# Kernel tuning notes

Measured on AMD Instinct MI355X. Metric: run time of the kernel, lower is better.

The kernel has to match this reference:

```python
import jax, jax.numpy as jnp
import numpy as np

IB = 8      # input/hidden activation bits
ABMVM = 8   # gate activation bits after MVM
ABNM = 8    # near-memory compute bits
NL = 0.05   # analog noise level
CY_DIV = 2.0
CY_SCALE = 2.0


def quant_pass(x, wb, sign):
    # Faithful port of QuantFunc.forward: clip/clamp then fake-quant (round to grid).
    if wb is None or wb == 0:
        return x
    if sign:
        delta = 0.0 if wb == 1 else 1.0 / (2.0 ** (wb - 1))
        x = jnp.clip(x, -1.0 + delta, 1.0 - delta)
    else:
        x = jnp.clip(x, 0.0, 1.0)
    if wb == 1:
        return jnp.sign(x)
    scale = 2.0 ** (wb - 1) if sign else 2.0 ** wb
    return jnp.round(x * scale) / scale


def setup_inputs() -> dict:
    key = jax.random.key(0)
    ks = jax.random.split(key, 7)
    B, I, H = 4096, 1024, 1024
    return {
        "input": jax.random.normal(ks[0], (B, I), jnp.float32),
        "hx": jax.random.normal(ks[1], (B, H), jnp.float32),
        "cx": jax.random.normal(ks[2], (B, H), jnp.float32),
        "weight_ih": jax.random.normal(ks[3], (4 * H, I), jnp.float32) * 0.1,
        "weight_hh": jax.random.normal(ks[4], (4 * H, H), jnp.float32) * 0.1,
        "bias_ih": jax.random.normal(ks[5], (4 * H,), jnp.float32) * 0.1,
        "bias_hh": jax.random.normal(ks[6], (4 * H,), jnp.float32) * 0.1,
        "train": 0,
    }


def reference(input, hx, cx, weight_ih, weight_hh, bias_ih, bias_hh, train):
    # Per-call Gaussian noise (simulated analog hardware); fixed key for reproducibility.
    nk = jax.random.split(jax.random.key(42), 4)
    noise_w_ih = jax.random.normal(nk[0], weight_ih.T.shape, weight_ih.dtype) * weight_ih.max() * NL
    noise_w_hh = jax.random.normal(nk[1], weight_hh.T.shape, weight_hh.dtype) * weight_hh.max() * NL
    noise_b_ih = jax.random.normal(nk[2], bias_ih.shape, bias_ih.dtype) * bias_ih.max() * NL
    noise_b_hh = jax.random.normal(nk[3], bias_hh.shape, bias_hh.dtype) * bias_hh.max() * NL

    # gates: [B, 4H]
    gates = (quant_pass(input, IB, True) @ (weight_ih.T + noise_w_ih) + bias_ih + noise_b_ih
             + quant_pass(hx, IB, True) @ (weight_hh.T + noise_w_hh) + bias_hh + noise_b_hh)

    ingate, forgetgate, cellgate, outgate = jnp.split(gates, 4, axis=1)
    ingate = quant_pass(jax.nn.sigmoid(ingate), ABMVM, False)
    forgetgate = quant_pass(jax.nn.sigmoid(forgetgate), ABMVM, False)
    cellgate = quant_pass(jnp.tanh(cellgate), ABMVM, True)
    outgate = quant_pass(jax.nn.sigmoid(outgate), ABMVM, False)

    cy = quant_pass((quant_pass(forgetgate * cx, ABNM, True)
                     + quant_pass(ingate * cellgate, ABNM, True)) / CY_DIV, ABNM, True)
    hy = quant_pass(outgate * quant_pass(jnp.tanh(cy * CY_SCALE), ABNM, True), ABNM, True)
    return (hy, cy)
```

## Files before the change

kernel.cpp:

```cpp
#include <hip/hip_runtime.h>
#include <hip/hip_bf16.h>
#include <stdint.h>
#include <stddef.h>


#define PART 1

typedef __attribute__((ext_vector_type(8))) short bf16x8;
typedef __attribute__((ext_vector_type(4))) float f32x4;

#define BATCH 4096

#define WS_A_OFF    ((size_t)0)
#define WS_B_OFF    ((size_t)16 << 20)
#define WS_BIAS_OFF ((size_t)48 << 20)
#define WS_MAX_OFF  (WS_BIAS_OFF + 16384)

__host__ __device__ inline void tf2x32(uint32_t k0, uint32_t k1,
                                       uint32_t x0, uint32_t x1,
                                       uint32_t &o0, uint32_t &o1)
{
  const uint32_t k2 = k0 ^ k1 ^ 0x1BD11BDAu;
#define TFR(r) { x0 += x1; x1 = (x1 << (r)) | (x1 >> (32 - (r))); x1 ^= x0; }
  x0 += k0; x1 += k1;
  TFR(13) TFR(15) TFR(26) TFR(6)
  x0 += k1; x1 += k2 + 1u;
  TFR(17) TFR(29) TFR(16) TFR(24)
  x0 += k2; x1 += k0 + 2u;
  TFR(13) TFR(15) TFR(26) TFR(6)
  x0 += k0; x1 += k1 + 3u;
  TFR(17) TFR(29) TFR(16) TFR(24)
  x0 += k1; x1 += k2 + 4u;
  TFR(13) TFR(15) TFR(26) TFR(6)
  x0 += k2; x1 += k0 + 5u;
#undef TFR
  o0 = x0; o1 = x1;
}

__device__ inline uint32_t jax_bits32(uint32_t k0, uint32_t k1, uint32_t i, uint32_t size)
{
#if PART
  uint32_t a, b;
  tf2x32(k0, k1, 0u, i, a, b);
  return a ^ b;
#else
  uint32_t half = size >> 1, a, b;
  if (i < half) { tf2x32(k0, k1, i, i + half, a, b); return a; }
  tf2x32(k0, k1, i - half, i, a, b); return b;
#endif
}

__device__ inline float bits_to_normal(uint32_t bits)
{
  float f = __uint_as_float((bits >> 9) | 0x3F800000u) - 1.0f;
  const float lo = -0x1.fffffep-1f;
  float u = fmaxf(lo, f * 2.0f + lo);
  float w = -log1pf(-u * u);
  float p;
  if (w < 5.0f) {
    w -= 2.5f;
    p = 2.81022636e-08f;
    p = fmaf(p, w, 3.43273939e-07f);
    p = fmaf(p, w, -3.5233877e-06f);
    p = fmaf(p, w, -4.39150654e-06f);
    p = fmaf(p, w, 0.00021858087f);
    p = fmaf(p, w, -0.00125372503f);
    p = fmaf(p, w, -0.00417768164f);
    p = fmaf(p, w, 0.246640727f);
    p = fmaf(p, w, 1.50140941f);
  } else {
    w = sqrtf(w) - 3.0f;
    p = -0.000200214257f;
    p = fmaf(p, w, 0.000100950558f);
    p = fmaf(p, w, 0.00134934322f);
    p = fmaf(p, w, -0.00367342844f);
    p = fmaf(p, w, 0.00573950773f);
    p = fmaf(p, w, -0.0076224613f);
    p = fmaf(p, w, 0.00943887047f);
    p = fmaf(p, w, 1.00167406f);
    p = fmaf(p, w, 2.83297682f);
  }
  return 0x1.6a09e6p+0f * (p * u);
}

__device__ inline float quantS8(float x)
{
  x = fminf(fmaxf(x, -0.9921875f), 0.9921875f);
  return rintf(x * 128.0f) * 0.0078125f;
}
__device__ inline float quantU8(float x)
{
  x = fminf(fmaxf(x, 0.0f), 1.0f);
  return rintf(x * 256.0f) * 0.00390625f;
}

#define LOG2E 1.44269504088896340736f
__device__ inline float sigmoid_fast(float x)
{
  float e = __builtin_amdgcn_exp2f(x * -LOG2E);
  return __builtin_amdgcn_rcpf(1.0f + e);
}
__device__ inline float tanh_fast(float x)
{
  float a = fabsf(x);
  float e = __builtin_amdgcn_exp2f(a * (-2.0f * LOG2E));
  float t = (1.0f - e) * __builtin_amdgcn_rcpf(1.0f + e);
  return copysignf(t, x);
}

__device__ inline unsigned short f2bf(float x)
{
  uint32_t b = __float_as_uint(x);
  return (unsigned short)((b + 0x7FFFu + ((b >> 16) & 1u)) >> 16);
}
__device__ inline float bf2f(unsigned short u) { return __uint_as_float(((uint32_t)u) << 16); }

__device__ inline float dec_max(uint32_t u)
{
  uint32_t bits = (u & 0x80000000u) ? (u ^ 0x80000000u) : ~u;
  return __uint_as_float(bits);
}

__global__ void init_max(uint32_t* mx)
{
  if (threadIdx.x < 4) mx[threadIdx.x] = 0u;
}

__global__ void kmax_all(const float4* __restrict__ wih, const float4* __restrict__ whh,
                         const float4* __restrict__ bih, const float4* __restrict__ bhh,
                         uint32_t* __restrict__ mx)
{
  const int blk = blockIdx.x;
  const float4* src; int n4, bl, nb; uint32_t* out;
  if (blk < 1024)      { src = wih; n4 = 1048576; bl = blk;        nb = 1024; out = mx + 0; }
  else if (blk < 2048) { src = whh; n4 = 1048576; bl = blk - 1024; nb = 1024; out = mx + 1; }
  else if (blk < 2052) { src = bih; n4 = 1024;    bl = blk - 2048; nb = 4;    out = mx + 2; }
  else                 { src = bhh; n4 = 1024;    bl = blk - 2052; nb = 4;    out = mx + 3; }

  float m = -3.4e38f;
  for (int i = bl * 256 + threadIdx.x; i < n4; i += nb * 256) {
    float4 v = src[i];
    m = fmaxf(fmaxf(m, fmaxf(v.x, v.y)), fmaxf(v.z, v.w));
  }
  for (int off = 32; off; off >>= 1) m = fmaxf(m, __shfl_down(m, off, 64));
  __shared__ float sm[4];
  if ((threadIdx.x & 63) == 0) sm[threadIdx.x >> 6] = m;
  __syncthreads();
  if (threadIdx.x == 0) {
    float bm = fmaxf(fmaxf(sm[0], sm[1]), fmaxf(sm[2], sm[3]));
    uint32_t bits = __float_as_uint(bm);
    uint32_t enc = (bits & 0x80000000u) ? ~bits : (bits | 0x80000000u);
    atomicMax(out, enc);
  }
}

__global__ void build_all(const float* __restrict__ wih, const float* __restrict__ whh,
                          const float4* __restrict__ in, const float4* __restrict__ hxp,
                          const float* __restrict__ bih, const float* __restrict__ bhh,
                          unsigned short* __restrict__ A, unsigned short* __restrict__ B,
                          float* __restrict__ biasE, const uint32_t* __restrict__ mxenc,
                          uint32_t kih0, uint32_t kih1, uint32_t khh0, uint32_t khh1,
                          uint32_t kbi0, uint32_t kbi1, uint32_t kbh0, uint32_t kbh1)
{
  const uint32_t blk = blockIdx.x;
  if (blk < 32768u) {
    uint32_t t = blk * 256u + threadIdx.x;
    uint32_t arr = t >> 22;
    uint32_t r = t & 4194303u;
    uint32_t k = r & 1023u;
    uint32_t n = r >> 10;
    const float* w = arr ? whh : wih;
    float mx = dec_max(mxenc[arr]);
    uint32_t key0 = arr ? khh0 : kih0, key1 = arr ? khh1 : kih1;
    uint32_t i = k * 4096u + n;
    float nrm = bits_to_normal(jax_bits32(key0, key1, i, 4194304u));
    float weff = w[(size_t)n * 1024u + k] + (nrm * mx) * 0.05f;
    unsigned short hi = f2bf(weff);
    unsigned short lob = f2bf(weff - bf2f(hi));
    uint32_t np = (n & 1023u) * 4u + (n >> 10);
    size_t base = (size_t)np * 4096u + (arr ? 1024u : 0u) + k;
    B[base] = hi;
    B[base + 2048u] = lob;
  } else if (blk < 40960u) {
    int t = (int)(blk - 32768u) * 256 + threadIdx.x;
    int b = t >> 9;
    int kq = t & 511;
    float4 v = (kq < 256) ? in[b * 256 + kq] : hxp[b * 256 + (kq - 256)];
    unsigned short o[4];
    o[0] = f2bf(quantS8(v.x)); o[1] = f2bf(quantS8(v.y));
    o[2] = f2bf(quantS8(v.z)); o[3] = f2bf(quantS8(v.w));
    *reinterpret_cast<uint64_t*>(A + (size_t)t * 4) = *reinterpret_cast<uint64_t*>(o);
  } else {
    uint32_t j = (blk - 40960u) * 256u + threadIdx.x;
    float mi = dec_max(mxenc[2]), mh = dec_max(mxenc[3]);
    float ni = (bits_to_normal(jax_bits32(kbi0, kbi1, j, 4096u)) * mi) * 0.05f;
    float nh = (bits_to_normal(jax_bits32(kbh0, kbh1, j, 4096u)) * mh) * 0.05f;
    biasE[(j & 1023u) * 4u + (j >> 10)] = ((bih[j] + ni) + bhh[j]) + nh;
  }
}

__device__ __forceinline__ void gload_lds16(const void* g, void* l)
{
  __builtin_amdgcn_global_load_lds((__attribute__((address_space(1))) void*)g,
                                   (__attribute__((address_space(3))) void*)l, 16, 0, 0);
}

#define VM0  asm volatile("s_waitcnt vmcnt(0)" ::: "memory")
#define NOVM
#define SBAR __builtin_amdgcn_s_barrier()
#define SCB  __builtin_amdgcn_sched_barrier(0)

#define BUFSZ 32768

#define STAGE_A(ts_, bi_)                                                         \
    { unsigned char* la_ = lds + (bi_) * BUFSZ; const int ka_ = (ts_) * 32;       \
      gload_lds16(Ar0 + ka_, la_ + tid * 16);                                     \
      gload_lds16(Ar1 + ka_, la_ + 4096 + tid * 16);                              \
      gload_lds16(Ar2 + ka_, la_ + 8192 + tid * 16);                              \
      gload_lds16(Ar3 + ka_, la_ + 12288 + tid * 16); }
#define STAGE_BH(ts_, bi_)                                                        \
    { unsigned char* la_ = lds + (bi_) * BUFSZ; const int ka_ = (ts_) * 32;       \
      gload_lds16(Br0 + ka_, la_ + 16384 + tid * 16);                             \
      gload_lds16(Br1 + ka_, la_ + 16384 + 4096 + tid * 16); }
#define STAGE_BL(ts_, bi_)                                                        \
    { unsigned char* la_ = lds + (bi_) * BUFSZ; const int ka_ = (ts_) * 32;       \
      gload_lds16(Br0 + 2048 + ka_, la_ + 24576 + tid * 16);                      \
      gload_lds16(Br1 + 2048 + ka_, la_ + 24576 + 4096 + tid * 16); }

#define TILE_ONE(t_, BUF_, BUFN_, DO_STAGE_, VM_ASM_)                             \
  {                                                                               \
    const unsigned char* pa_  = lds + (BUF_) * BUFSZ + aoff;                      \
    const unsigned char* pbh_ = lds + (BUF_) * BUFSZ + 16384 + boffU;             \
    const unsigned char* pbl_ = lds + (BUF_) * BUFSZ + 24576 + boffU;             \
    bf16x8 bh_[4], bl_[4], afL_[4], afH_[4];                                      \
    _Pragma("unroll") for (int n_ = 0; n_ < 4; ++n_)                              \
      bh_[n_] = *(const bf16x8*)(pbh_ + n_ * 1024);                               \
    _Pragma("unroll") for (int m_ = 0; m_ < 4; ++m_)                              \
      afL_[m_] = *(const bf16x8*)(pa_ + m_ * 1024);                               \
    if (DO_STAGE_) { STAGE_A((t_) + 1, BUFN_); }                                  \
    __builtin_amdgcn_s_setprio(1);                                                \
    _Pragma("unroll") for (int m_ = 0; m_ < 4; ++m_)                              \
      _Pragma("unroll") for (int n_ = 0; n_ < 4; ++n_)                            \
        acc[m_][n_] = __builtin_amdgcn_mfma_f32_16x16x32_bf16(afL_[m_], bh_[n_],  \
                                                              acc[m_][n_], 0, 0, 0); \
    __builtin_amdgcn_s_setprio(0);                                                \
    _Pragma("unroll") for (int m_ = 0; m_ < 4; ++m_)                              \
      afH_[m_] = *(const bf16x8*)(pa_ + (4 + m_) * 1024);                         \
    if (DO_STAGE_) { STAGE_BH((t_) + 1, BUFN_); }                                 \
    __builtin_amdgcn_s_setprio(1);                                                \
    _Pragma("unroll") for (int m_ = 0; m_ < 4; ++m_)                              \
      _Pragma("unroll") for (int n_ = 0; n_ < 4; ++n_)                            \
        acc[4 + m_][n_] = __builtin_amdgcn_mfma_f32_16x16x32_bf16(afH_[m_], bh_[n_], \
                                                              acc[4 + m_][n_], 0, 0, 0); \
    __builtin_amdgcn_s_setprio(0);                                                \
    _Pragma("unroll") for (int n_ = 0; n_ < 4; ++n_)                              \
      bl_[n_] = *(const bf16x8*)(pbl_ + n_ * 1024);                               \
    if (DO_STAGE_) { STAGE_BL((t_) + 1, BUFN_); }                                 \
    __builtin_amdgcn_s_setprio(1);                                                \
    _Pragma("unroll") for (int m_ = 0; m_ < 4; ++m_)                              \
      _Pragma("unroll") for (int n_ = 0; n_ < 4; ++n_)                            \
        acc[m_][n_] = __builtin_amdgcn_mfma_f32_16x16x32_bf16(afL_[m_], bl_[n_],  \
                                                              acc[m_][n_], 0, 0, 0); \
    _Pragma("unroll") for (int m_ = 0; m_ < 4; ++m_)                              \
      _Pragma("unroll") for (int n_ = 0; n_ < 4; ++n_)                            \
        acc[4 + m_][n_] = __builtin_amdgcn_mfma_f32_16x16x32_bf16(afH_[m_], bl_[n_], \
                                                              acc[4 + m_][n_], 0, 0, 0); \
    __builtin_amdgcn_s_setprio(0);                                                \
    VM_ASM_;                                                                      \
    SBAR; SCB;                                                                    \
  }

#define LTS 136

__global__ __launch_bounds__(256, 2) void gemm_gates(
    const unsigned short* __restrict__ A,
    const unsigned short* __restrict__ B,
    const float* __restrict__ bias,
    const float* __restrict__ cx,
    float* __restrict__ hy,
    float* __restrict__ cy)
{
  extern __shared__ unsigned char lds[];
  const int tid  = threadIdx.x;
  const int lane = tid & 63;
  const int wave = tid >> 6;
  const int wr = wave >> 1;
  const int wc = wave & 1;

  const int bid = blockIdx.x;
  const int wg  = (bid & 7) * 64 + (bid >> 3);
  const int brow = (wg & 15) * 256;
  const int bcol = (wg >> 4) * 128;

#define CHUNK_SRC(c_, sr_, sk_) \
    { int p_ = (c_) >> 3, lc_ = ((c_) & 7) ^ (p_ & 7); \
      sr_ = p_ * 2 + (lc_ >> 2); sk_ = (lc_ & 3) * 8; }
  int sr, sk;
  CHUNK_SRC(tid,        sr, sk);
  const unsigned short* Ar0 = A + (size_t)(brow + sr) * 2048 + sk;
  const unsigned short* Br0 = B + (size_t)(bcol + sr) * 4096 + sk;
  CHUNK_SRC(tid + 256,  sr, sk);
  const unsigned short* Ar1 = A + (size_t)(brow + sr) * 2048 + sk;
  const unsigned short* Br1 = B + (size_t)(bcol + sr) * 4096 + sk;
  CHUNK_SRC(tid + 512,  sr, sk);
  const unsigned short* Ar2 = A + (size_t)(brow + sr) * 2048 + sk;
  CHUNK_SRC(tid + 768,  sr, sk);
  const unsigned short* Ar3 = A + (size_t)(brow + sr) * 2048 + sk;
#undef CHUNK_SRC

  const int lrh = (lane & 15) >> 1;
  const int chk = ((((lane & 1) << 2) | (lane >> 4)) ^ lrh);
  const int aoff  = wr * 8192 + lrh * 128 + chk * 16;
  const int boffU = wc * 4096 + lrh * 128 + chk * 16;

  f32x4 acc[8][4] = {};

  STAGE_A(0, 0); STAGE_BH(0, 0); STAGE_BL(0, 0);
  VM0;
  SBAR; SCB;

#pragma unroll 1
  for (int t = 0; t < 63; ++t) {
    TILE_ONE(t, (t & 1), ((t + 1) & 1), 1, VM0);
  }
  TILE_ONE(63, 1, 0, 0, NOVM);

  float* LT = (float*)lds;
  const int col_local0 = wc * 64 + (lane & 15);
  const int lrow = (lane >> 4) << 2;
  const int h = tid & 31;
  const int hg = (bcol >> 2) + h;

#pragma unroll
  for (int hh = 0; hh < 2; ++hh) {
    __syncthreads();
#pragma unroll
    for (int m = 0; m < 4; ++m) {
#pragma unroll
      for (int n = 0; n < 4; ++n) {
        const int cl = col_local0 + n * 16;
        const float bv = bias[bcol + cl];
        const int lr0 = wr * 64 + m * 16 + lrow;
#pragma unroll
        for (int r = 0; r < 4; ++r)
          LT[(lr0 + r) * LTS + cl] = acc[hh * 4 + m][n][r] + bv;
      }
    }
    __syncthreads();
#pragma unroll
    for (int i = 0; i < 16; ++i) {
      const int lr = (tid >> 5) * 16 + i;
      const int grow = brow + ((lr >> 6) << 7) + hh * 64 + (lr & 63);
      const float4 q = *(const float4*)(LT + lr * LTS + 4 * h);
      const size_t oidx = (size_t)grow * 1024 + hg;
      float ing = quantU8(sigmoid_fast(q.x));
      float fg  = quantU8(sigmoid_fast(q.y));
      float cg  = quantS8(tanh_fast(q.z));
      float og  = quantU8(sigmoid_fast(q.w));
      float c0  = cx[oidx];
      float cyv = quantS8((quantS8(fg * c0) + quantS8(ing * cg)) * 0.5f);
      float hyv = quantS8(og * quantS8(tanh_fast(cyv * 2.0f)));
      hy[oidx] = hyv;
      cy[oidx] = cyv;
    }
  }
}

extern "C" void kernel_launch(void* const* d_in, const int* in_sizes, int n_in,
                              void* d_out, int out_size, void* d_ws, size_t ws_size,
                              hipStream_t stream)
{
  const float* input = (const float*)d_in[0];
  const float* hx    = (const float*)d_in[1];
  const float* cx    = (const float*)d_in[2];
  const float* wih   = (const float*)d_in[3];
  const float* whh   = (const float*)d_in[4];
  const float* bih   = (const float*)d_in[5];
  const float* bhh   = (const float*)d_in[6];
  (void)in_sizes; (void)n_in; (void)ws_size;

  uint8_t* ws = (uint8_t*)d_ws;
  unsigned short* A   = (unsigned short*)(ws + WS_A_OFF);
  unsigned short* B   = (unsigned short*)(ws + WS_B_OFF);
  float* biasE        = (float*)(ws + WS_BIAS_OFF);
  uint32_t* mx        = (uint32_t*)(ws + WS_MAX_OFF);

  uint32_t nk[4][2];
#if PART
  for (int i = 0; i < 4; ++i) tf2x32(0u, 42u, 0u, (uint32_t)i, nk[i][0], nk[i][1]);
#else
  {
    uint32_t w0[4], w1[4];
    for (int i = 0; i < 4; ++i) tf2x32(0u, 42u, (uint32_t)i, (uint32_t)(i + 4), w0[i], w1[i]);
    uint32_t out8[8] = {w0[0], w0[1], w0[2], w0[3], w1[0], w1[1], w1[2], w1[3]};
    for (int i = 0; i < 4; ++i) { nk[i][0] = out8[2 * i]; nk[i][1] = out8[2 * i + 1]; }
  }
#endif

  init_max<<<1, 64, 0, stream>>>(mx);
  kmax_all<<<2056, 256, 0, stream>>>((const float4*)wih, (const float4*)whh,
                                     (const float4*)bih, (const float4*)bhh, mx);
  build_all<<<40976, 256, 0, stream>>>(wih, whh, (const float4*)input, (const float4*)hx,
                                       bih, bhh, A, B, biasE, mx,
                                       nk[0][0], nk[0][1], nk[1][0], nk[1][1],
                                       nk[2][0], nk[2][1], nk[3][0], nk[3][1]);

  float* hy = (float*)d_out;
  float* cyp = hy + (size_t)BATCH * 1024;

  (void)hipFuncSetAttribute((const void*)gemm_gates,
                            hipFuncAttributeMaxDynamicSharedMemorySize, 71680);
  gemm_gates<<<dim3(512), dim3(256), 71680, stream>>>(A, B, biasE, cx, hy, cyp);
}
```

Baseline: 191.5 us.

## Switch gate GEMM to 32x32x16 MFMA tiles and pack weight-build stores

Replaces the 16x16x32 bf16 MFMA inner loop with 32x32x16 MFMAs and reworks the LDS fragment offsets, swizzle, accumulator layout and epilogue row mapping to match. All next-tile staging is now issued at the start of each tile instead of being interleaved between MFMA groups. Separately, the weight-build kernel handles two k elements per thread and writes packed 32-bit hi/lo bf16 pairs, halving the grid size. The larger MFMA shape is meant to reduce LDS fragment reads per FLOP, at the cost of different register pressure and less overlap between staging and compute.

```diff
diff --git a/kernel.cpp b/kernel.cpp
--- a/kernel.cpp
+++ b/kernel.cpp
@@ -7,7 +7,7 @@
 #define PART 1
 
 typedef __attribute__((ext_vector_type(8))) short bf16x8;
-typedef __attribute__((ext_vector_type(4))) float f32x4;
+typedef __attribute__((ext_vector_type(16))) float f32x16;
 
 #define BATCH 4096
 
@@ -163,26 +163,33 @@
                           uint32_t kbi0, uint32_t kbi1, uint32_t kbh0, uint32_t kbh1)
 {
   const uint32_t blk = blockIdx.x;
-  if (blk < 32768u) {
+  if (blk < 16384u) {
     uint32_t t = blk * 256u + threadIdx.x;
-    uint32_t arr = t >> 22;
-    uint32_t r = t & 4194303u;
-    uint32_t k = r & 1023u;
-    uint32_t n = r >> 10;
+    uint32_t arr = t >> 21;
+    uint32_t r = t & 2097151u;
+    uint32_t kp = r & 511u;
+    uint32_t n = r >> 9;
     const float* w = arr ? whh : wih;
     float mx = dec_max(mxenc[arr]);
     uint32_t key0 = arr ? khh0 : kih0, key1 = arr ? khh1 : kih1;
-    uint32_t i = k * 4096u + n;
-    float nrm = bits_to_normal(jax_bits32(key0, key1, i, 4194304u));
-    float weff = w[(size_t)n * 1024u + k] + (nrm * mx) * 0.05f;
-    unsigned short hi = f2bf(weff);
-    unsigned short lob = f2bf(weff - bf2f(hi));
+    uint32_t k0 = kp * 2u;
+    uint32_t hiw = 0u, low = 0u;
+#pragma unroll
+    for (int e = 0; e < 2; ++e) {
+      uint32_t k = k0 + (uint32_t)e;
+      float nrm = bits_to_normal(jax_bits32(key0, key1, k * 4096u + n, 4194304u));
+      float weff = w[(size_t)n * 1024u + k] + (nrm * mx) * 0.05f;
+      unsigned short hi = f2bf(weff);
+      unsigned short lob = f2bf(weff - bf2f(hi));
+      hiw |= ((uint32_t)hi) << (16 * e);
+      low |= ((uint32_t)lob) << (16 * e);
+    }
     uint32_t np = (n & 1023u) * 4u + (n >> 10);
-    size_t base = (size_t)np * 4096u + (arr ? 1024u : 0u) + k;
-    B[base] = hi;
-    B[base + 2048u] = lob;
-  } else if (blk < 40960u) {
-    int t = (int)(blk - 32768u) * 256 + threadIdx.x;
+    size_t base = (size_t)np * 4096u + (arr ? 1024u : 0u) + k0;
+    *reinterpret_cast<uint32_t*>(B + base) = hiw;
+    *reinterpret_cast<uint32_t*>(B + base + 2048u) = low;
+  } else if (blk < 24576u) {
+    int t = (int)(blk - 16384u) * 256 + threadIdx.x;
     int b = t >> 9;
     int kq = t & 511;
     float4 v = (kq < 256) ? in[b * 256 + kq] : hxp[b * 256 + (kq - 256)];
@@ -191,7 +198,7 @@
     o[2] = f2bf(quantS8(v.z)); o[3] = f2bf(quantS8(v.w));
     *reinterpret_cast<uint64_t*>(A + (size_t)t * 4) = *reinterpret_cast<uint64_t*>(o);
   } else {
-    uint32_t j = (blk - 40960u) * 256u + threadIdx.x;
+    uint32_t j = (blk - 24576u) * 256u + threadIdx.x;
     float mi = dec_max(mxenc[2]), mh = dec_max(mxenc[3]);
     float ni = (bits_to_normal(jax_bits32(kbi0, kbi1, j, 4096u)) * mi) * 0.05f;
     float nh = (bits_to_normal(jax_bits32(kbh0, kbh1, j, 4096u)) * mh) * 0.05f;
@@ -229,42 +236,43 @@
 
 #define TILE_ONE(t_, BUF_, BUFN_, DO_STAGE_, VM_ASM_)                             \
   {                                                                               \
-    const unsigned char* pa_  = lds + (BUF_) * BUFSZ + aoff;                      \
-    const unsigned char* pbh_ = lds + (BUF_) * BUFSZ + 16384 + boffU;             \
-    const unsigned char* pbl_ = lds + (BUF_) * BUFSZ + 24576 + boffU;             \
-    bf16x8 bh_[4], bl_[4], afL_[4], afH_[4];                                      \
-    _Pragma("unroll") for (int n_ = 0; n_ < 4; ++n_)                              \
-      bh_[n_] = *(const bf16x8*)(pbh_ + n_ * 1024);                               \
-    _Pragma("unroll") for (int m_ = 0; m_ < 4; ++m_)                              \
-      afL_[m_] = *(const bf16x8*)(pa_ + m_ * 1024);                               \
-    if (DO_STAGE_) { STAGE_A((t_) + 1, BUFN_); }                                  \
+    const unsigned char* pa_  = lds + (BUF_) * BUFSZ;                             \
+    const unsigned char* pbh_ = lds + (BUF_) * BUFSZ + 16384 + wcB;               \
+    const unsigned char* pbl_ = lds + (BUF_) * BUFSZ + 24576 + wcB;               \
+    bf16x8 a0_[4], a1_[4], bh0_[2], bh1_[2], bl0_[2], bl1_[2];                    \
+    if (DO_STAGE_) { STAGE_A((t_) + 1, BUFN_); STAGE_BH((t_) + 1, BUFN_);         \
+                     STAGE_BL((t_) + 1, BUFN_); }                                 \
+    _Pragma("unroll") for (int n_ = 0; n_ < 2; ++n_)                              \
+      bh0_[n_] = *(const bf16x8*)(pbh_ + off0 + n_ * 2048);                       \
+    _Pragma("unroll") for (int m_ = 0; m_ < 4; ++m_)                              \
+      a0_[m_] = *(const bf16x8*)(pa_ + aoff0 + m_ * 2048);                        \
+    _Pragma("unroll") for (int m_ = 0; m_ < 4; ++m_)                              \
+      a1_[m_] = *(const bf16x8*)(pa_ + aoff1 + m_ * 2048);                        \
+    _Pragma("unroll") for (int n_ = 0; n_ < 2; ++n_)                              \
+      bh1_[n_] = *(const bf16x8*)(pbh_ + off1 + n_ * 2048);                       \
     __builtin_amdgcn_s_setprio(1);                                                \
     _Pragma("unroll") for (int m_ = 0; m_ < 4; ++m_)                              \
-      _Pragma("unroll") for (int n_ = 0; n_ < 4; ++n_)                            \
-        acc[m_][n_] = __builtin_amdgcn_mfma_f32_16x16x32_bf16(afL_[m_], bh_[n_],  \
+      _Pragma("unroll") for (int n_ = 0; n_ < 2; ++n_)                            \
+        acc[m_][n_] = __builtin_amdgcn_mfma_f32_32x32x16_bf16(a0_[m_], bh0_[n_],  \
                                                               acc[m_][n_], 0, 0, 0); \
     __builtin_amdgcn_s_setprio(0);                                                \
-    _Pragma("unroll") for (int m_ = 0; m_ < 4; ++m_)                              \
-      afH_[m_] = *(const bf16x8*)(pa_ + (4 + m_) * 1024);                         \
-    if (DO_STAGE_) { STAGE_BH((t_) + 1, BUFN_); }                                 \
+    _Pragma("unroll") for (int n_ = 0; n_ < 2; ++n_)                              \
+      bl0_[n_] = *(const bf16x8*)(pbl_ + off0 + n_ * 2048);                       \
+    _Pragma("unroll") for (int n_ = 0; n_ < 2; ++n_)                              \
+      bl1_[n_] = *(const bf16x8*)(pbl_ + off1 + n_ * 2048);                       \
     __builtin_amdgcn_s_setprio(1);                                                \
     _Pragma("unroll") for (int m_ = 0; m_ < 4; ++m_)                              \
-      _Pragma("unroll") for (int n_ = 0; n_ < 4; ++n_)                            \
-        acc[4 + m_][n_] = __builtin_amdgcn_mfma_f32_16x16x32_bf16(afH_[m_], bh_[n_], \
-                                                              acc[4 + m_][n_], 0, 0, 0); \
-    __builtin_amdgcn_s_setprio(0);                                                \
-    _Pragma("unroll") for (int n_ = 0; n_ < 4; ++n_)                              \
-      bl_[n_] = *(const bf16x8*)(pbl_ + n_ * 1024);                               \
-    if (DO_STAGE_) { STAGE_BL((t_) + 1, BUFN_); }                                 \
-    __builtin_amdgcn_s_setprio(1);                                                \
-    _Pragma("unroll") for (int m_ = 0; m_ < 4; ++m_)                              \
-      _Pragma("unroll") for (int n_ = 0; n_ < 4; ++n_)                            \
-        acc[m_][n_] = __builtin_amdgcn_mfma_f32_16x16x32_bf16(afL_[m_], bl_[n_],  \
+      _Pragma("unroll") for (int n_ = 0; n_ < 2; ++n_)                            \
+        acc[m_][n_] = __builtin_amdgcn_mfma_f32_32x32x16_bf16(a1_[m_], bh1_[n_],  \
                                                               acc[m_][n_], 0, 0, 0); \
     _Pragma("unroll") for (int m_ = 0; m_ < 4; ++m_)                              \
-      _Pragma("unroll") for (int n_ = 0; n_ < 4; ++n_)                            \
-        acc[4 + m_][n_] = __builtin_amdgcn_mfma_f32_16x16x32_bf16(afH_[m_], bl_[n_], \
-                                                              acc[4 + m_][n_], 0, 0, 0); \
+      _Pragma("unroll") for (int n_ = 0; n_ < 2; ++n_)                            \
+        acc[m_][n_] = __builtin_amdgcn_mfma_f32_32x32x16_bf16(a0_[m_], bl0_[n_],  \
+                                                              acc[m_][n_], 0, 0, 0); \
+    _Pragma("unroll") for (int m_ = 0; m_ < 4; ++m_)                              \
+      _Pragma("unroll") for (int n_ = 0; n_ < 2; ++n_)                            \
+        acc[m_][n_] = __builtin_amdgcn_mfma_f32_32x32x16_bf16(a1_[m_], bl1_[n_],  \
+                                                              acc[m_][n_], 0, 0, 0); \
     __builtin_amdgcn_s_setprio(0);                                                \
     VM_ASM_;                                                                      \
     SBAR; SCB;                                                                    \
@@ -308,12 +316,17 @@
   const unsigned short* Ar3 = A + (size_t)(brow + sr) * 2048 + sk;
 #undef CHUNK_SRC
 
-  const int lrh = (lane & 15) >> 1;
-  const int chk = ((((lane & 1) << 2) | (lane >> 4)) ^ lrh);
-  const int aoff  = wr * 8192 + lrh * 128 + chk * 16;
-  const int boffU = wc * 4096 + lrh * 128 + chk * 16;
-
-  f32x4 acc[8][4] = {};
+  const int lrh = (lane & 31) >> 1;
+  const int cbase = ((lane & 1) << 2) | (lane >> 5);
+  const int chk0 = (cbase)     ^ (lrh & 7);
+  const int chk1 = (cbase | 2) ^ (lrh & 7);
+  const int aoff0 = wr * 8192 + lrh * 128 + chk0 * 16;
+  const int aoff1 = wr * 8192 + lrh * 128 + chk1 * 16;
+  const int off0  = lrh * 128 + chk0 * 16;
+  const int off1  = lrh * 128 + chk1 * 16;
+  const int wcB   = wc * 4096;
+
+  f32x16 acc[4][2] = {};
 
   STAGE_A(0, 0); STAGE_BH(0, 0); STAGE_BL(0, 0);
   VM0;
@@ -326,8 +339,8 @@
   TILE_ONE(63, 1, 0, 0, NOVM);
 
   float* LT = (float*)lds;
-  const int col_local0 = wc * 64 + (lane & 15);
-  const int lrow = (lane >> 4) << 2;
+  const int cl0 = wc * 64 + (lane & 31);
+  const int rbase = wr * 64 + ((lane >> 5) << 2);
   const int h = tid & 31;
   const int hg = (bcol >> 2) + h;
 
@@ -335,22 +348,24 @@
   for (int hh = 0; hh < 2; ++hh) {
     __syncthreads();
 #pragma unroll
-    for (int m = 0; m < 4; ++m) {
-#pragma unroll
-      for (int n = 0; n < 4; ++n) {
-        const int cl = col_local0 + n * 16;
+    for (int mm = 0; mm < 2; ++mm) {
+#pragma unroll
+      for (int n = 0; n < 2; ++n) {
+        const int cl = cl0 + n * 32;
         const float bv = bias[bcol + cl];
-        const int lr0 = wr * 64 + m * 16 + lrow;
-#pragma unroll
-        for (int r = 0; r < 4; ++r)
-          LT[(lr0 + r) * LTS + cl] = acc[hh * 4 + m][n][r] + bv;
+#pragma unroll
+        for (int reg = 0; reg < 16; ++reg) {
+          const int rl = rbase + mm * 32 + (reg & 3) + ((reg >> 2) << 3);
+          LT[rl * LTS + cl] = acc[hh * 2 + mm][n][reg] + bv;
+        }
       }
     }
     __syncthreads();
 #pragma unroll
     for (int i = 0; i < 16; ++i) {
       const int lr = (tid >> 5) * 16 + i;
-      const int grow = brow + ((lr >> 6) << 7) + hh * 64 + (lr & 63);
+      const int grow = brow + ((lr >> 6) << 7) + (hh * 2 + ((lr >> 5) & 1)) * 32
+                       + (lr & 31);
       const float4 q = *(const float4*)(LT + lr * LTS + 4 * h);
       const size_t oidx = (size_t)grow * 1024 + hg;
       float ing = quantU8(sigmoid_fast(q.x));
@@ -400,7 +415,7 @@
   init_max<<<1, 64, 0, stream>>>(mx);
   kmax_all<<<2056, 256, 0, stream>>>((const float4*)wih, (const float4*)whh,
                                      (const float4*)bih, (const float4*)bhh, mx);
-  build_all<<<40976, 256, 0, stream>>>(wih, whh, (const float4*)input, (const float4*)hx,
+  build_all<<<24592, 256, 0, stream>>>(wih, whh, (const float4*)input, (const float4*)hx,
                                        bih, bhh, A, B, biasE, mx,
                                        nk[0][0], nk[0][1], nk[1][0], nk[1][1],
                                        nk[2][0], nk[2][1], nk[3][0], nk[3][1]);
```

Measured after the change: 214.8 us. 12.2% more time.
